# Kernel optimization log

Hardware: AMD Instinct MI355X
Metric: run time of the kernel (lower is better)

## Reference

```python
import jax, jax.numpy as jnp
import numpy as np

B, N, D_IN, D_OUT = 4, 2048, 4096, 4096
E, R, D_ATT = 8, 16, 128
SCALING = 16.0 / 16.0  # alpha / rank


def setup_inputs() -> dict:
    key = jax.random.key(0)
    ks = jax.random.split(key, 8)
    x = jax.random.normal(ks[0], (B, N, D_IN), dtype=jnp.float32)
    weight = jax.random.normal(ks[1], (D_OUT, D_IN), dtype=jnp.float32) * 0.02  # frozen base
    bias = jax.random.normal(ks[2], (D_OUT,), dtype=jnp.float32) * 0.02
    router_V = jax.random.normal(ks[3], (D_ATT, D_IN), dtype=jnp.float32) * 0.02
    router_U = jax.random.normal(ks[4], (D_ATT, D_IN), dtype=jnp.float32) * 0.02
    router_W = jax.random.normal(ks[5], (E, D_ATT), dtype=jnp.float32) * 0.02
    experts_A = jax.random.normal(ks[6], (E, D_IN, R), dtype=jnp.float32) * 0.01
    experts_B = jax.random.normal(ks[7], (E, R, D_OUT), dtype=jnp.float32) * 0.01
    return {"x": x, "weight": weight, "bias": bias, "router_V": router_V,
            "router_U": router_U, "router_W": router_W,
            "experts_A": experts_A, "experts_B": experts_B}


def reference(x, weight, bias, router_V, router_U, router_W, experts_A, experts_B):
    # Frozen base projection: F.linear(x, weight, bias)
    base = jnp.einsum('bnd,od->bno', x, weight) + bias
    # ABMIL gated-attention router
    v = jnp.tanh(jnp.einsum('bnd,ad->bna', x, router_V))            # [B,N,D_att]
    u = jax.nn.sigmoid(jnp.einsum('bnd,ad->bna', x, router_U))      # [B,N,D_att]
    scores = jnp.einsum('bna,ea->bne', v * u, router_W)             # [B,N,E]
    router_weights = jax.nn.sigmoid(scores)                         # independent sigmoid gates
    # Per-expert low-rank path (dropout is identity at inference / p=0)
    lora_down = jnp.einsum('bnd,edr->bner', x, experts_A)           # [B,N,E,R]
    weighted = lora_down * router_weights[..., None]
    moe_out = jnp.einsum('bner,erd->bnd', weighted, experts_B)      # [B,N,D_out]
    return base + SCALING * moe_out
```

## Files before the change

kernel.cpp:

```cpp
#include <hip/hip_runtime.h>
#include <hip/hip_bf16.h>

#define M_TOT   8192
#define D_IN    4096
#define D_OUT   4096
#define N_E     8
#define N_R     16
#define D_ATT   128
#define ER      128
#define CATN    384
#define KEXT    4224
#define NTK     66
#define NTM     32

typedef __attribute__((ext_vector_type(8))) __bf16 bf16x8;
typedef __attribute__((ext_vector_type(4))) float  f32x4;

__device__ __forceinline__ ushort f2bf(float f) {
  union { float f; unsigned u; } v; v.f = f;
  unsigned r = (v.u + 0x7fffu + ((v.u >> 16) & 1u)) >> 16;
  return (ushort)r;
}

__global__ void f2bf4_kernel(const float* __restrict__ in, ushort* __restrict__ out, long n4) {
  long i = blockIdx.x * (long)blockDim.x + threadIdx.x;
  if (i >= n4) return;
  const float4 a = reinterpret_cast<const float4*>(in)[i];
  ushort4 r; r.x = f2bf(a.x); r.y = f2bf(a.y); r.z = f2bf(a.z); r.w = f2bf(a.w);
  reinterpret_cast<ushort4*>(out)[i] = r;
}

__global__ void f2bf4s_kernel(const float* __restrict__ in, ushort* __restrict__ out, long n4) {
  long i = blockIdx.x * (long)blockDim.x + threadIdx.x;
  if (i >= n4) return;
  const float4 a = reinterpret_cast<const float4*>(in)[i];
  ushort4 r; r.x = f2bf(a.x); r.y = f2bf(a.y); r.z = f2bf(a.z); r.w = f2bf(a.w);
  long row = i >> 10, c4 = (i & 1023) << 2;
  *reinterpret_cast<ushort4*>(out + row * KEXT + c4) = r;
}

__global__ void prep_catA_kernel(const float* __restrict__ expA, ushort* __restrict__ cat) {
  int idx = blockIdx.x * 256 + threadIdx.x;
  int j = idx >> 12, d = idx & 4095;
  int e = j >> 4, r = j & 15;
  cat[(size_t)(2 * D_ATT + j) * D_IN + d] = f2bf(expA[((size_t)e * D_IN + d) * N_R + r]);
}

__global__ void prep_bt_kernel(const float* __restrict__ expB, ushort* __restrict__ we) {
  int idx = blockIdx.x * 256 + threadIdx.x;
  int j = idx >> 12, o = idx & 4095;
  we[(size_t)o * KEXT + D_IN + j] = f2bf(expB[(size_t)j * D_OUT + o]);
}

__global__ void gate_kernel(const float* __restrict__ P, const float* __restrict__ rW,
                            ushort* __restrict__ wtd) {
  int token = blockIdx.x * 4 + (threadIdx.x >> 6);
  int l = threadIdx.x & 63;
  const float* p = P + (size_t)token * CATN;
  float v0 = tanhf(p[l]);
  float v1 = tanhf(p[l + 64]);
  float u0 = 1.f / (1.f + __expf(-p[D_ATT + l]));
  float u1 = 1.f / (1.f + __expf(-p[D_ATT + l + 64]));
  float g0 = v0 * u0, g1 = v1 * u1;
  float rw[8];
  #pragma unroll
  for (int e = 0; e < 8; ++e) {
    float s = g0 * rW[e * D_ATT + l] + g1 * rW[e * D_ATT + l + 64];
    #pragma unroll
    for (int off = 32; off > 0; off >>= 1) s += __shfl_xor(s, off);
    rw[e] = 1.f / (1.f + __expf(-s));
  }
  int q = l >> 4;
  float rw_a = (q == 0) ? rw[0] : (q == 1) ? rw[1] : (q == 2) ? rw[2] : rw[3];
  float rw_b = (q == 0) ? rw[4] : (q == 1) ? rw[5] : (q == 2) ? rw[6] : rw[7];
  wtd[(size_t)token * KEXT + l]      = f2bf(p[2 * D_ATT + l]      * rw_a);
  wtd[(size_t)token * KEXT + l + 64] = f2bf(p[2 * D_ATT + l + 64] * rw_b);
}

__global__ __launch_bounds__(256, 2)
void gemm128_kernel(const ushort* __restrict__ A, const ushort* __restrict__ Bm,
                    float* __restrict__ C)
{
  __shared__ ushort As[128 * 64];
  __shared__ ushort Bs[128 * 64];
  const int tid = threadIdx.x;
  const int w = tid >> 6, l = tid & 63;
  const int wr = w >> 1, wc = w & 1;
  const int l16 = l & 15, lq = l >> 4;
  const int brow = blockIdx.y * 128;
  const int bcol = blockIdx.x * 128;

  f32x4 acc[4][4] = {};

  for (int kt = 0; kt < (D_IN >> 6); ++kt) {
    int k0 = kt << 6;
    #pragma unroll
    for (int c = 0; c < 4; ++c) {
      int rloc = w * 32 + c * 8;
      int rl = rloc + (l >> 3);
      int kk = k0 + (l & 7) * 8;
      const ushort* ga = A  + (size_t)(brow + rl) * KEXT + kk;
      const ushort* gb = Bm + (size_t)(bcol + rl) * D_IN + kk;
      __builtin_amdgcn_global_load_lds((const __attribute__((address_space(1))) void*)ga,
                                       (__attribute__((address_space(3))) void*)(As + rloc * 64),
                                       16, 0, 0);
      __builtin_amdgcn_global_load_lds((const __attribute__((address_space(1))) void*)gb,
                                       (__attribute__((address_space(3))) void*)(Bs + rloc * 64),
                                       16, 0, 0);
    }
    __syncthreads();

    #pragma unroll
    for (int ks = 0; ks < 2; ++ks) {
      bf16x8 af[4], bfv[4];
      #pragma unroll
      for (int mi = 0; mi < 4; ++mi)
        af[mi] = *reinterpret_cast<const bf16x8*>(As + (wr * 64 + mi * 16 + l16) * 64 + ks * 32 + lq * 8);
      #pragma unroll
      for (int ni = 0; ni < 4; ++ni)
        bfv[ni] = *reinterpret_cast<const bf16x8*>(Bs + (wc * 64 + ni * 16 + l16) * 64 + ks * 32 + lq * 8);
      #pragma unroll
      for (int mi = 0; mi < 4; ++mi)
        #pragma unroll
        for (int ni = 0; ni < 4; ++ni)
          acc[mi][ni] = __builtin_amdgcn_mfma_f32_16x16x32_bf16(af[mi], bfv[ni], acc[mi][ni], 0, 0, 0);
    }
    __syncthreads();
  }

  #pragma unroll
  for (int ni = 0; ni < 4; ++ni) {
    int col = bcol + wc * 64 + ni * 16 + l16;
    #pragma unroll
    for (int mi = 0; mi < 4; ++mi) {
      f32x4 v = acc[mi][ni];
      int row0 = brow + wr * 64 + mi * 16 + lq * 4;
      #pragma unroll
      for (int j = 0; j < 4; ++j)
        C[(size_t)(row0 + j) * CATN + col] = v[j];
    }
  }
}

__global__ __launch_bounds__(512, 2)
void gemm256_kernel(const ushort* __restrict__ A, const ushort* __restrict__ Bm,
                    float* __restrict__ C, const float* __restrict__ bias)
{
  __shared__ ushort lds[2][2][2][8192];
  const int tid = threadIdx.x;
  const int wid = tid >> 6, l = tid & 63;
  const int wr = wid >> 2, wc = wid & 3;
  const int l16 = l & 15, lq = l >> 4;
  const int rxor = (l16 & 7) << 3;

  const int cpx = (NTM * (D_OUT / 256)) >> 3;
  const int sid = ((int)blockIdx.x & 7) * cpx + ((int)blockIdx.x >> 3);
  const int brow = (sid % NTM) * 256;
  const int bcol = (sid / NTM) * 256;

  const int srow = tid >> 3;
  const int scol = (((tid & 7) ^ ((tid >> 3) & 7)) << 3);

#define STAGE(buf_, mat_, half_, kt_) do {                                        \
    const ushort* _s = (mat_) ? Bm : A;                                           \
    int _rb = ((mat_) ? bcol : brow) + (half_) * 128 + srow;                      \
    ushort* _d = &lds[(buf_)][(mat_)][(half_)][wid * 512];                        \
    _Pragma("unroll")                                                             \
    for (int _c = 0; _c < 2; ++_c) {                                              \
      const ushort* _g = _s + (size_t)(_rb + _c * 64) * KEXT + (kt_) * 64 + scol; \
      __builtin_amdgcn_global_load_lds(                                           \
          (const __attribute__((address_space(1))) void*)_g,                      \
          (__attribute__((address_space(3))) void*)(_d + _c * 4096), 16, 0, 0);   \
    } } while (0)

#define LDA_FRAG(buf_, mi_, ks_) \
  (*reinterpret_cast<const bf16x8*>(&lds[(buf_)][0][wr][((mi_) * 16 + l16) * 64 + (((ks_) * 32 + lq * 8) ^ rxor)]))
#define LDB_FRAG(buf_, ni_, ks_) \
  (*reinterpret_cast<const bf16x8*>(&lds[(buf_)][1][wc >> 1][((wc & 1) * 64 + (ni_) * 16 + l16) * 64 + (((ks_) * 32 + lq * 8) ^ rxor)]))

#define RD_ALO(buf_, dst_) \
    _Pragma("unroll") for (int mi = 0; mi < 4; ++mi) \
      _Pragma("unroll") for (int ks = 0; ks < 2; ++ks) dst_[mi][ks] = LDA_FRAG(buf_, mi, ks);
#define RD_BLO(buf_, dst_) \
    _Pragma("unroll") for (int ni = 0; ni < 2; ++ni) \
      _Pragma("unroll") for (int ks = 0; ks < 2; ++ks) dst_[ni][ks] = LDB_FRAG(buf_, ni, ks);

#define MFMA_Q(accm0_, accn0_, a_, b_) \
    _Pragma("unroll") for (int mi = 0; mi < 4; ++mi) \
      _Pragma("unroll") for (int ni = 0; ni < 2; ++ni) \
        _Pragma("unroll") for (int ks = 0; ks < 2; ++ks) \
          acc[(accm0_) + mi][(accn0_) + ni] = __builtin_amdgcn_mfma_f32_16x16x32_bf16( \
              a_[mi][ks], b_[ni][ks], acc[(accm0_) + mi][(accn0_) + ni], 0, 0, 0);

#define TILE(t_, buf_, aIn_, b0In_, aOut_, b0Out_) do {                           \
    bf16x8 b1[2][2], aHi[4][2];                                                   \
    const int ktA = ((t_) + 1 < NTK) ? (t_) + 1 : NTK - 1;                        \
    const int ktB = ((t_) + 2 < NTK) ? (t_) + 2 : NTK - 1;                        \
                                                                          \
    STAGE(buf_ ^ 1, 0, 0, ktA);                                                   \
    __builtin_amdgcn_s_barrier();                                                 \
    asm volatile("s_waitcnt lgkmcnt(0)" ::: "memory");                            \
    __builtin_amdgcn_s_setprio(1);                                                \
    _Pragma("unroll") for (int ni = 0; ni < 2; ++ni)                              \
      _Pragma("unroll") for (int ks = 0; ks < 2; ++ks)                            \
        b1[ni][ks] = LDB_FRAG(buf_, ni + 2, ks);                                  \
    MFMA_Q(0, 0, aIn_, b0In_);                                                    \
    __builtin_amdgcn_s_setprio(0);                                                \
    __builtin_amdgcn_s_barrier();                                                 \
                                                                          \
    STAGE(buf_ ^ 1, 0, 1, ktA);                                                   \
    __builtin_amdgcn_s_barrier();                                                 \
    asm volatile("s_waitcnt lgkmcnt(0)" ::: "memory");                            \
    __builtin_amdgcn_s_setprio(1);                                                \
    _Pragma("unroll") for (int mi = 0; mi < 4; ++mi)                              \
      _Pragma("unroll") for (int ks = 0; ks < 2; ++ks)                            \
        aHi[mi][ks] = LDA_FRAG(buf_, mi + 4, ks);                                 \
    MFMA_Q(0, 2, aIn_, b1);                                                       \
    __builtin_amdgcn_s_setprio(0);                                                \
    __builtin_amdgcn_s_barrier();                                                 \
                                                                          \
    STAGE(buf_, 1, 0, ktB);                                                       \
    __builtin_amdgcn_s_barrier();                                                 \
    asm volatile("s_waitcnt lgkmcnt(0)" ::: "memory");                            \
    __builtin_amdgcn_s_setprio(1);                                                \
    MFMA_Q(4, 2, aHi, b1);                                                        \
    __builtin_amdgcn_s_setprio(0);                                                \
    __builtin_amdgcn_s_barrier();                                                 \
                                                                          \
    STAGE(buf_, 1, 1, ktB);                                                       \
    asm volatile("s_waitcnt vmcnt(4)" ::: "memory");                              \
    __builtin_amdgcn_s_barrier();                                                 \
    __builtin_amdgcn_s_setprio(1);                                                \
    RD_ALO(buf_ ^ 1, aOut_);                                                      \
    RD_BLO(buf_ ^ 1, b0Out_);                                                     \
    MFMA_Q(4, 0, aHi, b0In_);                                                     \
    __builtin_amdgcn_s_setprio(0);                                                \
    __builtin_amdgcn_s_barrier();                                                 \
  } while (0)

  f32x4 acc[8][4] = {};
  bf16x8 aA[4][2], b0A[2][2], aB[4][2], b0B[2][2];

  STAGE(0, 0, 0, 0); STAGE(0, 0, 1, 0);
  STAGE(0, 1, 0, 0); STAGE(0, 1, 1, 0);
  STAGE(1, 1, 0, 1); STAGE(1, 1, 1, 1);
  asm volatile("s_waitcnt vmcnt(4)" ::: "memory");
  __builtin_amdgcn_s_barrier();
  RD_ALO(0, aA);
  RD_BLO(0, b0A);

  #pragma unroll 1
  for (int tp = 0; tp < NTK / 2; ++tp) {
    TILE(2 * tp,     0, aA, b0A, aB, b0B);
    TILE(2 * tp + 1, 1, aB, b0B, aA, b0A);
  }

  asm volatile("s_waitcnt vmcnt(0) lgkmcnt(0)" ::: "memory");

  #pragma unroll
  for (int ni = 0; ni < 4; ++ni) {
    int col = bcol + wc * 64 + ni * 16 + l16;
    float bs = bias[col];
    #pragma unroll
    for (int mi = 0; mi < 8; ++mi) {
      int row0 = brow + wr * 128 + mi * 16 + lq * 4;
      #pragma unroll
      for (int j = 0; j < 4; ++j)
        C[(size_t)(row0 + j) * D_OUT + col] = acc[mi][ni][j] + bs;
    }
  }
#undef STAGE
#undef LDA_FRAG
#undef LDB_FRAG
#undef RD_ALO
#undef RD_BLO
#undef MFMA_Q
#undef TILE
}

extern "C" void kernel_launch(void* const* d_in, const int* in_sizes, int n_in,
                              void* d_out, int out_size, void* d_ws, size_t ws_size,
                              hipStream_t stream) {
  const float* x      = (const float*)d_in[0];
  const float* weight = (const float*)d_in[1];
  const float* bias   = (const float*)d_in[2];
  const float* rV     = (const float*)d_in[3];
  const float* rU     = (const float*)d_in[4];
  const float* rW     = (const float*)d_in[5];
  const float* expA   = (const float*)d_in[6];
  const float* expB   = (const float*)d_in[7];
  float* out = (float*)d_out;

  ushort* xe  = (ushort*)d_ws;
  ushort* we  = xe  + (size_t)M_TOT * KEXT;
  ushort* cat = we  + (size_t)D_OUT * KEXT;
  float*  P   = (float*)(cat + (size_t)CATN * D_IN);

  long n4;
  n4 = (long)M_TOT * D_IN / 4;
  f2bf4s_kernel<<<dim3((n4 + 255) / 256), 256, 0, stream>>>(x, xe, n4);
  n4 = (long)D_OUT * D_IN / 4;
  f2bf4s_kernel<<<dim3((n4 + 255) / 256), 256, 0, stream>>>(weight, we, n4);
  n4 = (long)D_ATT * D_IN / 4;
  f2bf4_kernel<<<dim3((n4 + 255) / 256), 256, 0, stream>>>(rV, cat, n4);
  f2bf4_kernel<<<dim3((n4 + 255) / 256), 256, 0, stream>>>(rU, cat + (size_t)D_ATT * D_IN, n4);
  prep_catA_kernel<<<dim3(ER * D_IN / 256), 256, 0, stream>>>(expA, cat);
  prep_bt_kernel<<<dim3(ER * D_OUT / 256), 256, 0, stream>>>(expB, we);

  gemm128_kernel<<<dim3(CATN / 128, M_TOT / 128), 256, 0, stream>>>(xe, cat, P);

  gate_kernel<<<dim3(M_TOT / 4), 256, 0, stream>>>(P, rW, xe + D_IN);

  gemm256_kernel<<<dim3((D_OUT / 256) * (M_TOT / 256)), 512, 0, stream>>>(xe, we, out, bias);
}
```

Baseline: 401.4 us.

## Switch main GEMM to 32x32x16 MFMA tiles and remap block-to-tile order

The 256x256 main GEMM now uses 32x32x16 bf16 MFMA instructions instead of 16x16x32. Fragment loads, accumulator layout (f32x16) and the epilogue store mapping change to match. Larger MFMA tiles cut the number of LDS fragment reads and MFMA issues per unit of work, raising arithmetic intensity per instruction. The block-to-tile mapping also changes to a per-XCD 8x8 grouped layout meant to improve L2 locality. The risks are a mismatched LDS swizzle causing bank conflicts and more strided output stores.

```diff
diff --git a/kernel.cpp b/kernel.cpp
--- a/kernel.cpp
+++ b/kernel.cpp
@@ -13,8 +13,9 @@
 #define NTK     66
 #define NTM     32
 
-typedef __attribute__((ext_vector_type(8))) __bf16 bf16x8;
-typedef __attribute__((ext_vector_type(4))) float  f32x4;
+typedef __attribute__((ext_vector_type(8)))  __bf16 bf16x8;
+typedef __attribute__((ext_vector_type(4)))  float  f32x4;
+typedef __attribute__((ext_vector_type(16))) float  f32x16;
 
 __device__ __forceinline__ ushort f2bf(float f) {
   union { float f; unsigned u; } v; v.f = f;
@@ -150,13 +151,12 @@
   const int tid = threadIdx.x;
   const int wid = tid >> 6, l = tid & 63;
   const int wr = wid >> 2, wc = wid & 3;
-  const int l16 = l & 15, lq = l >> 4;
-  const int rxor = (l16 & 7) << 3;
-
-  const int cpx = (NTM * (D_OUT / 256)) >> 3;
-  const int sid = ((int)blockIdx.x & 7) * cpx + ((int)blockIdx.x >> 3);
-  const int brow = (sid % NTM) * 256;
-  const int bcol = (sid / NTM) * 256;
+  const int l31 = l & 31, hi8 = (l >> 5) * 8;
+  const int rxor = (l & 7) << 3;
+
+  const int xcd = (int)blockIdx.x & 7, q = (int)blockIdx.x >> 3;
+  const int brow = ((xcd >> 1) * 8 + (q >> 3)) * 256;
+  const int bcol = ((xcd & 1) * 8 + (q & 7)) * 256;
 
   const int srow = tid >> 3;
   const int scol = (((tid & 7) ^ ((tid >> 3) & 7)) << 3);
@@ -173,81 +173,75 @@
           (__attribute__((address_space(3))) void*)(_d + _c * 4096), 16, 0, 0);   \
     } } while (0)
 
-#define LDA_FRAG(buf_, mi_, ks_) \
-  (*reinterpret_cast<const bf16x8*>(&lds[(buf_)][0][wr][((mi_) * 16 + l16) * 64 + (((ks_) * 32 + lq * 8) ^ rxor)]))
-#define LDB_FRAG(buf_, ni_, ks_) \
-  (*reinterpret_cast<const bf16x8*>(&lds[(buf_)][1][wc >> 1][((wc & 1) * 64 + (ni_) * 16 + l16) * 64 + (((ks_) * 32 + lq * 8) ^ rxor)]))
-
-#define RD_ALO(buf_, dst_) \
-    _Pragma("unroll") for (int mi = 0; mi < 4; ++mi) \
-      _Pragma("unroll") for (int ks = 0; ks < 2; ++ks) dst_[mi][ks] = LDA_FRAG(buf_, mi, ks);
-#define RD_BLO(buf_, dst_) \
-    _Pragma("unroll") for (int ni = 0; ni < 2; ++ni) \
-      _Pragma("unroll") for (int ks = 0; ks < 2; ++ks) dst_[ni][ks] = LDB_FRAG(buf_, ni, ks);
-
-#define MFMA_Q(accm0_, accn0_, a_, b_) \
-    _Pragma("unroll") for (int mi = 0; mi < 4; ++mi) \
-      _Pragma("unroll") for (int ni = 0; ni < 2; ++ni) \
-        _Pragma("unroll") for (int ks = 0; ks < 2; ++ks) \
-          acc[(accm0_) + mi][(accn0_) + ni] = __builtin_amdgcn_mfma_f32_16x16x32_bf16( \
-              a_[mi][ks], b_[ni][ks], acc[(accm0_) + mi][(accn0_) + ni], 0, 0, 0);
+#define LDA32(buf_, mt_, ks_) \
+  (*reinterpret_cast<const bf16x8*>(&lds[(buf_)][0][wr][((mt_) * 32 + l31) * 64 + ((((ks_) * 16) + hi8) ^ rxor)]))
+#define LDB32(buf_, nt_, ks_) \
+  (*reinterpret_cast<const bf16x8*>(&lds[(buf_)][1][wc >> 1][((wc & 1) * 64 + (nt_) * 32 + l31) * 64 + ((((ks_) * 16) + hi8) ^ rxor)]))
+
+#define RD32_A(buf_, mb_, dst_) \
+    _Pragma("unroll") for (int mt = 0; mt < 2; ++mt) \
+      _Pragma("unroll") for (int ks = 0; ks < 4; ++ks) dst_[mt][ks] = LDA32(buf_, (mb_) + mt, ks);
+#define RD32_B(buf_, nt_, dst_) \
+    _Pragma("unroll") for (int ks = 0; ks < 4; ++ks) dst_[ks] = LDB32(buf_, nt_, ks);
+
+#define MFMA_Q32(mb_, n_, a_, b_) \
+    _Pragma("unroll") for (int ks = 0; ks < 4; ++ks) \
+      _Pragma("unroll") for (int mt = 0; mt < 2; ++mt) \
+        acc[(mb_) + mt][n_] = __builtin_amdgcn_mfma_f32_32x32x16_bf16( \
+            a_[mt][ks], b_[ks], acc[(mb_) + mt][n_], 0, 0, 0);
 
 #define TILE(t_, buf_, aIn_, b0In_, aOut_, b0Out_) do {                           \
-    bf16x8 b1[2][2], aHi[4][2];                                                   \
+    bf16x8 b1[4], aHi[2][4];                                                      \
     const int ktA = ((t_) + 1 < NTK) ? (t_) + 1 : NTK - 1;                        \
     const int ktB = ((t_) + 2 < NTK) ? (t_) + 2 : NTK - 1;                        \
-                                                                          \
+                                                  \
     STAGE(buf_ ^ 1, 0, 0, ktA);                                                   \
     __builtin_amdgcn_s_barrier();                                                 \
     asm volatile("s_waitcnt lgkmcnt(0)" ::: "memory");                            \
     __builtin_amdgcn_s_setprio(1);                                                \
-    _Pragma("unroll") for (int ni = 0; ni < 2; ++ni)                              \
-      _Pragma("unroll") for (int ks = 0; ks < 2; ++ks)                            \
-        b1[ni][ks] = LDB_FRAG(buf_, ni + 2, ks);                                  \
-    MFMA_Q(0, 0, aIn_, b0In_);                                                    \
+    RD32_B(buf_, 1, b1);                                                          \
+    MFMA_Q32(0, 0, aIn_, b0In_);                                                  \
     __builtin_amdgcn_s_setprio(0);                                                \
     __builtin_amdgcn_s_barrier();                                                 \
-                                                                          \
+                                                  \
     STAGE(buf_ ^ 1, 0, 1, ktA);                                                   \
     __builtin_amdgcn_s_barrier();                                                 \
     asm volatile("s_waitcnt lgkmcnt(0)" ::: "memory");                            \
     __builtin_amdgcn_s_setprio(1);                                                \
-    _Pragma("unroll") for (int mi = 0; mi < 4; ++mi)                              \
-      _Pragma("unroll") for (int ks = 0; ks < 2; ++ks)                            \
-        aHi[mi][ks] = LDA_FRAG(buf_, mi + 4, ks);                                 \
-    MFMA_Q(0, 2, aIn_, b1);                                                       \
+    RD32_A(buf_, 2, aHi);                                                         \
+    MFMA_Q32(0, 1, aIn_, b1);                                                     \
     __builtin_amdgcn_s_setprio(0);                                                \
     __builtin_amdgcn_s_barrier();                                                 \
-                                                                          \
+                                                            \
     STAGE(buf_, 1, 0, ktB);                                                       \
     __builtin_amdgcn_s_barrier();                                                 \
     asm volatile("s_waitcnt lgkmcnt(0)" ::: "memory");                            \
     __builtin_amdgcn_s_setprio(1);                                                \
-    MFMA_Q(4, 2, aHi, b1);                                                        \
+    MFMA_Q32(2, 1, aHi, b1);                                                      \
     __builtin_amdgcn_s_setprio(0);                                                \
     __builtin_amdgcn_s_barrier();                                                 \
-                                                                          \
+                                          \
     STAGE(buf_, 1, 1, ktB);                                                       \
     asm volatile("s_waitcnt vmcnt(4)" ::: "memory");                              \
     __builtin_amdgcn_s_barrier();                                                 \
     __builtin_amdgcn_s_setprio(1);                                                \
-    RD_ALO(buf_ ^ 1, aOut_);                                                      \
-    RD_BLO(buf_ ^ 1, b0Out_);                                                     \
-    MFMA_Q(4, 0, aHi, b0In_);                                                     \
+    RD32_A(buf_ ^ 1, 0, aOut_);                                                   \
+    RD32_B(buf_ ^ 1, 0, b0Out_);                                                  \
+    MFMA_Q32(2, 0, aHi, b0In_);                                                   \
     __builtin_amdgcn_s_setprio(0);                                                \
     __builtin_amdgcn_s_barrier();                                                 \
   } while (0)
 
-  f32x4 acc[8][4] = {};
-  bf16x8 aA[4][2], b0A[2][2], aB[4][2], b0B[2][2];
+  f32x16 acc[4][2] = {};
+  bf16x8 aA[2][4], b0A[4], aB[2][4], b0B[4];
 
   STAGE(0, 0, 0, 0); STAGE(0, 0, 1, 0);
   STAGE(0, 1, 0, 0); STAGE(0, 1, 1, 0);
   STAGE(1, 1, 0, 1); STAGE(1, 1, 1, 1);
   asm volatile("s_waitcnt vmcnt(4)" ::: "memory");
   __builtin_amdgcn_s_barrier();
-  RD_ALO(0, aA);
-  RD_BLO(0, b0A);
+  RD32_A(0, 0, aA);
+  RD32_B(0, 0, b0A);
 
   #pragma unroll 1
   for (int tp = 0; tp < NTK / 2; ++tp) {
@@ -258,23 +252,26 @@
   asm volatile("s_waitcnt vmcnt(0) lgkmcnt(0)" ::: "memory");
 
   #pragma unroll
-  for (int ni = 0; ni < 4; ++ni) {
-    int col = bcol + wc * 64 + ni * 16 + l16;
+  for (int nt = 0; nt < 2; ++nt) {
+    int col = bcol + wc * 64 + nt * 32 + l31;
     float bs = bias[col];
     #pragma unroll
-    for (int mi = 0; mi < 8; ++mi) {
-      int row0 = brow + wr * 128 + mi * 16 + lq * 4;
-      #pragma unroll
-      for (int j = 0; j < 4; ++j)
-        C[(size_t)(row0 + j) * D_OUT + col] = acc[mi][ni][j] + bs;
+    for (int mt = 0; mt < 4; ++mt) {
+      f32x16 v = acc[mt][nt];
+      int row0 = brow + wr * 128 + mt * 32 + 4 * (l >> 5);
+      #pragma unroll
+      for (int reg = 0; reg < 16; ++reg) {
+        int row = row0 + (reg & 3) + 8 * (reg >> 2);
+        C[(size_t)row * D_OUT + col] = v[reg] + bs;
+      }
     }
   }
 #undef STAGE
-#undef LDA_FRAG
-#undef LDB_FRAG
-#undef RD_ALO
-#undef RD_BLO
-#undef MFMA_Q
+#undef LDA32
+#undef LDB32
+#undef RD32_A
+#undef RD32_B
+#undef MFMA_Q32
 #undef TILE
 }
 
```

New measurement: 407.1 us. No clear change (+1.4%).

## Split-K the router GEMM with bf16 partials and retile the main GEMM's block mapping

Applied to the files above, without the earlier changes.

The router/LoRA-down GEMM is split into two K halves along grid z, doubling its block count from 192 to 384 so more CUs are busy. Each half writes a bf16 partial that the gate kernel sums, which cuts the partial-output write traffic. The main GEMM's block-to-tile mapping is changed so each XCD handles a contiguous 8x8 patch of tiles, aiming for better L2 reuse. The cost is precision loss from rounding the router pre-activations and LoRA-down values to bf16, plus an extra partial read in the gate kernel.

```diff
diff --git a/kernel.cpp b/kernel.cpp
--- a/kernel.cpp
+++ b/kernel.cpp
@@ -11,15 +11,18 @@
 #define CATN    384
 #define KEXT    4224
 #define NTK     66
-#define NTM     32
-
-typedef __attribute__((ext_vector_type(8))) __bf16 bf16x8;
-typedef __attribute__((ext_vector_type(4))) float  f32x4;
+
+typedef __attribute__((ext_vector_type(8)))  __bf16 bf16x8;
+typedef __attribute__((ext_vector_type(4)))  float  f32x4;
 
 __device__ __forceinline__ ushort f2bf(float f) {
   union { float f; unsigned u; } v; v.f = f;
   unsigned r = (v.u + 0x7fffu + ((v.u >> 16) & 1u)) >> 16;
   return (ushort)r;
+}
+__device__ __forceinline__ float bf2f(ushort u) {
+  union { unsigned u; float f; } v; v.u = ((unsigned)u) << 16;
+  return v.f;
 }
 
 __global__ void f2bf4_kernel(const float* __restrict__ in, ushort* __restrict__ out, long n4) {
@@ -52,15 +55,16 @@
   we[(size_t)o * KEXT + D_IN + j] = f2bf(expB[(size_t)j * D_OUT + o]);
 }
 
-__global__ void gate_kernel(const float* __restrict__ P, const float* __restrict__ rW,
+__global__ void gate_kernel(const ushort* __restrict__ P, const float* __restrict__ rW,
                             ushort* __restrict__ wtd) {
   int token = blockIdx.x * 4 + (threadIdx.x >> 6);
   int l = threadIdx.x & 63;
-  const float* p = P + (size_t)token * CATN;
-  float v0 = tanhf(p[l]);
-  float v1 = tanhf(p[l + 64]);
-  float u0 = 1.f / (1.f + __expf(-p[D_ATT + l]));
-  float u1 = 1.f / (1.f + __expf(-p[D_ATT + l + 64]));
+  const ushort* p0 = P + (size_t)token * CATN;
+  const ushort* p1 = p0 + (size_t)M_TOT * CATN;
+  float v0 = tanhf(bf2f(p0[l])      + bf2f(p1[l]));
+  float v1 = tanhf(bf2f(p0[l + 64]) + bf2f(p1[l + 64]));
+  float u0 = 1.f / (1.f + __expf(-(bf2f(p0[D_ATT + l])      + bf2f(p1[D_ATT + l]))));
+  float u1 = 1.f / (1.f + __expf(-(bf2f(p0[D_ATT + l + 64]) + bf2f(p1[D_ATT + l + 64]))));
   float g0 = v0 * u0, g1 = v1 * u1;
   float rw[8];
   #pragma unroll
@@ -73,13 +77,15 @@
   int q = l >> 4;
   float rw_a = (q == 0) ? rw[0] : (q == 1) ? rw[1] : (q == 2) ? rw[2] : rw[3];
   float rw_b = (q == 0) ? rw[4] : (q == 1) ? rw[5] : (q == 2) ? rw[6] : rw[7];
-  wtd[(size_t)token * KEXT + l]      = f2bf(p[2 * D_ATT + l]      * rw_a);
-  wtd[(size_t)token * KEXT + l + 64] = f2bf(p[2 * D_ATT + l + 64] * rw_b);
+  float lo_a = bf2f(p0[2 * D_ATT + l])      + bf2f(p1[2 * D_ATT + l]);
+  float lo_b = bf2f(p0[2 * D_ATT + l + 64]) + bf2f(p1[2 * D_ATT + l + 64]);
+  wtd[(size_t)token * KEXT + l]      = f2bf(lo_a * rw_a);
+  wtd[(size_t)token * KEXT + l + 64] = f2bf(lo_b * rw_b);
 }
 
 __global__ __launch_bounds__(256, 2)
 void gemm128_kernel(const ushort* __restrict__ A, const ushort* __restrict__ Bm,
-                    float* __restrict__ C)
+                    ushort* __restrict__ C)
 {
   __shared__ ushort As[128 * 64];
   __shared__ ushort Bs[128 * 64];
@@ -89,10 +95,11 @@
   const int l16 = l & 15, lq = l >> 4;
   const int brow = blockIdx.y * 128;
   const int bcol = blockIdx.x * 128;
+  const int kt0 = (int)blockIdx.z << 5;
 
   f32x4 acc[4][4] = {};
 
-  for (int kt = 0; kt < (D_IN >> 6); ++kt) {
+  for (int kt = kt0; kt < kt0 + 32; ++kt) {
     int k0 = kt << 6;
     #pragma unroll
     for (int c = 0; c < 4; ++c) {
@@ -128,6 +135,7 @@
     __syncthreads();
   }
 
+  ushort* Cz = C + (size_t)blockIdx.z * M_TOT * CATN;
   #pragma unroll
   for (int ni = 0; ni < 4; ++ni) {
     int col = bcol + wc * 64 + ni * 16 + l16;
@@ -137,7 +145,7 @@
       int row0 = brow + wr * 64 + mi * 16 + lq * 4;
       #pragma unroll
       for (int j = 0; j < 4; ++j)
-        C[(size_t)(row0 + j) * CATN + col] = v[j];
+        Cz[(size_t)(row0 + j) * CATN + col] = f2bf(v[j]);
     }
   }
 }
@@ -153,10 +161,9 @@
   const int l16 = l & 15, lq = l >> 4;
   const int rxor = (l16 & 7) << 3;
 
-  const int cpx = (NTM * (D_OUT / 256)) >> 3;
-  const int sid = ((int)blockIdx.x & 7) * cpx + ((int)blockIdx.x >> 3);
-  const int brow = (sid % NTM) * 256;
-  const int bcol = (sid / NTM) * 256;
+  const int xcd = (int)blockIdx.x & 7, q = (int)blockIdx.x >> 3;
+  const int brow = ((xcd >> 1) * 8 + (q >> 3)) * 256;
+  const int bcol = ((xcd & 1) * 8 + (q & 7)) * 256;
 
   const int srow = tid >> 3;
   const int scol = (((tid & 7) ^ ((tid >> 3) & 7)) << 3);
@@ -294,7 +301,7 @@
   ushort* xe  = (ushort*)d_ws;
   ushort* we  = xe  + (size_t)M_TOT * KEXT;
   ushort* cat = we  + (size_t)D_OUT * KEXT;
-  float*  P   = (float*)(cat + (size_t)CATN * D_IN);
+  ushort* P   = cat + (size_t)CATN * D_IN;
 
   long n4;
   n4 = (long)M_TOT * D_IN / 4;
@@ -307,7 +314,7 @@
   prep_catA_kernel<<<dim3(ER * D_IN / 256), 256, 0, stream>>>(expA, cat);
   prep_bt_kernel<<<dim3(ER * D_OUT / 256), 256, 0, stream>>>(expB, we);
 
-  gemm128_kernel<<<dim3(CATN / 128, M_TOT / 128), 256, 0, stream>>>(xe, cat, P);
+  gemm128_kernel<<<dim3(CATN / 128, M_TOT / 128, 2), 256, 0, stream>>>(xe, cat, P);
 
   gate_kernel<<<dim3(M_TOT / 4), 256, 0, stream>>>(P, rW, xe + D_IN);
 
```

Measured after the change: 354.8 us. -11.6%, faster.
